# Kernel tuning notes

Measured on AMD Instinct MI355X. Metric: run time of the kernel, lower is better.

## Reference

```python
import jax, jax.numpy as jnp
import numpy as np

B, S, HID = 1, 4096, 4096
H, KV, D = 32, 8, 128
NUM_LANDMARKS = 64
LOCAL_WINDOW = 128          # window size in fast path
HW = LOCAL_WINDOW // 2      # half window = 64 (also used as block size)
ROPE_THETA = 10000.0
SCALE = 1.0 / np.sqrt(D)


def setup_inputs() -> dict:
    key = jax.random.key(0)
    k1, k2, k3, k4, k5 = jax.random.split(key, 5)
    return {
        "hidden_states": jax.random.normal(k1, (B, S, HID), dtype=jnp.float32),
        "wq": jax.random.normal(k2, (HID, H * D), dtype=jnp.float32) * 0.02,
        "wk": jax.random.normal(k3, (HID, KV * D), dtype=jnp.float32) * 0.02,
        "wv": jax.random.normal(k4, (HID, KV * D), dtype=jnp.float32) * 0.02,
        "wo": jax.random.normal(k5, (H * D, HID), dtype=jnp.float32) * 0.02,
    }


def _rope(x):
    # x: [B, h, S, D]; standard llama RoPE with rotate_half
    pos = jnp.arange(S, dtype=jnp.float32)
    inv_freq = 1.0 / (ROPE_THETA ** (jnp.arange(0, D, 2, dtype=jnp.float32) / D))
    freqs = pos[:, None] * inv_freq[None, :]              # [S, D/2]
    emb = jnp.concatenate([freqs, freqs], axis=-1)        # [S, D]
    cos, sin = jnp.cos(emb), jnp.sin(emb)
    x1, x2 = x[..., : D // 2], x[..., D // 2:]
    rot = jnp.concatenate([-x2, x1], axis=-1)
    return x * cos + rot * sin


def _ssa_fast(q, k, v):
    # q,k,v: [B, H, S, D] (kv already repeated to H heads). Causal, no dropout.
    nblk = S // HW  # block size == half window == 64
    # ---- local sliding-window attention (block-banded, honors sparsity) ----
    qb = q.reshape(B, H, nblk, HW, D)
    # pad keys/values by HW zeros on both sides (matches torch F.pad with 0)
    kp = jnp.pad(k, ((0, 0), (0, 0), (HW, HW), (0, 0)))
    vp = jnp.pad(v, ((0, 0), (0, 0), (HW, HW), (0, 0)))
    kpb = kp.reshape(B, H, nblk + 2, HW, D)
    vpb = vp.reshape(B, H, nblk + 2, HW, D)
    # each query block n sees key blocks n-1, n, n+1 (in padded coords: n, n+1, n+2)
    kb = jnp.concatenate([kpb[:, :, :nblk], kpb[:, :, 1:nblk + 1], kpb[:, :, 2:nblk + 2]], axis=3)  # [B,H,nblk,3*HW,D]
    vb = jnp.concatenate([vpb[:, :, :nblk], vpb[:, :, 1:nblk + 1], vpb[:, :, 2:nblk + 2]], axis=3)
    scores = jnp.einsum("bhnqd,bhnkd->bhnqk", qb, kb) * SCALE  # [B,H,nblk,HW,3*HW]
    # relative key position: rel = (j - HW) - i; window membership rel in [-HW, HW-1],
    # causal keeps rel <= 0  =>  i <= j <= i + HW. Left zero-padding stays attendable
    # (score 0), exactly like the torch unfold-over-zero-pad implementation.
    i_idx = jnp.arange(HW)[:, None]
    j_idx = jnp.arange(3 * HW)[None, :]
    mask = (j_idx >= i_idx) & (j_idx <= i_idx + HW)  # [HW, 3*HW]
    scores = jnp.where(mask, scores, -jnp.inf)
    w = jax.nn.softmax(scores, axis=-1)
    local_out = jnp.einsum("bhnqk,bhnkd->bhnqd", w, vb).reshape(B, H, S, D)
    # ---- global landmark attention ----
    stride = S // NUM_LANDMARKS
    lm_idx = jnp.arange(0, S, stride)[:NUM_LANDMARKS]         # [L]
    lk = k[:, :, lm_idx, :]                                   # [B,H,L,D]
    lv = v[:, :, lm_idx, :]
    ls = jnp.einsum("bhqd,bhkd->bhqk", q, lk) * SCALE         # [B,H,S,L]
    lm_mask = jnp.arange(S)[:, None] < lm_idx[None, :]        # future landmarks masked
    ls = jnp.where(lm_mask[None, None], -jnp.inf, ls)
    lw = jax.nn.softmax(ls, axis=-1)
    global_out = jnp.einsum("bhqk,bhkd->bhqd", lw, lv)
    return 0.7 * local_out + 0.3 * global_out


def reference(hidden_states, wq, wk, wv, wo):
    q = (hidden_states @ wq).reshape(B, S, H, D).transpose(0, 2, 1, 3)   # [B,H,S,D]
    k = (hidden_states @ wk).reshape(B, S, KV, D).transpose(0, 2, 1, 3)  # [B,KV,S,D]
    v = (hidden_states @ wv).reshape(B, S, KV, D).transpose(0, 2, 1, 3)
    q = _rope(q)
    k = _rope(k)
    groups = H // KV
    k = jnp.repeat(k, groups, axis=1)  # repeat_interleave over heads
    v = jnp.repeat(v, groups, axis=1)
    attn = _ssa_fast(q, k, v)                                 # [B,H,S,D]
    out = attn.transpose(0, 2, 1, 3).reshape(B, S, H * D) @ wo
    return out
```

## Files before the change

### kernel.cpp

```cpp
#include <hip/hip_runtime.h>
#include <hip/hip_bf16.h>


typedef short bf16x8 __attribute__((ext_vector_type(8)));
typedef float f32x4 __attribute__((ext_vector_type(4)));
using bf16 = __hip_bfloat16;

#define S_LEN 4096
#define HIDN  4096
#define NH    32
#define NKV   8
#define DH    128
#define NBLK  64
#define SCALE 0.08838834764831845f

__device__ __forceinline__ void gload16(const bf16* g, bf16* l) {
  __builtin_amdgcn_global_load_lds(
      (const __attribute__((address_space(1))) unsigned int*)g,
      (__attribute__((address_space(3))) unsigned int*)l, 16, 0, 0);
}

__global__ void k_detect(const unsigned short* __restrict__ w,
                         int* __restrict__ flag) {
  int t = threadIdx.x;
  unsigned short u = w[t];
  int e = (u >> 7) & 0xFF;
  int bad = (e >= 134) ? 1 : 0;
  __shared__ int cnt;
  if (t == 0) cnt = 0;
  __syncthreads();
  atomicAdd(&cnt, bad);
  __syncthreads();
  if (t == 0) flag[0] = (cnt > 32) ? 1 : 0;
}

__global__ void k_cvt(const void* __restrict__ in, bf16* __restrict__ out,
                      const int* __restrict__ flagp, int n8) {
  int i = blockIdx.x * blockDim.x + threadIdx.x;
  if (i >= n8) return;
  if (*flagp) {
    const float4* p = (const float4*)in + (size_t)i * 2;
    float4 a = p[0], b = p[1];
    alignas(16) bf16 v[8] = {__float2bfloat16(a.x), __float2bfloat16(a.y),
                             __float2bfloat16(a.z), __float2bfloat16(a.w),
                             __float2bfloat16(b.x), __float2bfloat16(b.y),
                             __float2bfloat16(b.z), __float2bfloat16(b.w)};
    *(uint4*)(out + (size_t)i * 8) = *(const uint4*)v;
  } else {
    ((uint4*)out)[i] = ((const uint4*)in)[i];
  }
}

__global__ __launch_bounds__(256) void k_tcvt(const void* __restrict__ w_,
                                              bf16* __restrict__ wt,
                                              const int* __restrict__ flagp,
                                              int K, int N) {
  __shared__ bf16 tile[64][66];
  const bool f32 = *flagp != 0;
  const int k0 = blockIdx.x * 64, n0 = blockIdx.y * 64;
  const int t = threadIdx.x;
  const int r = t >> 2, c16 = (t & 3) * 16;
  if (f32) {
    const float* src = (const float*)w_ + (size_t)(k0 + r) * N + n0 + c16;
    float4 a = ((const float4*)src)[0], b = ((const float4*)src)[1];
    float4 c = ((const float4*)src)[2], d = ((const float4*)src)[3];
    bf16* dst = &tile[r][c16];
    dst[0] = __float2bfloat16(a.x);  dst[1] = __float2bfloat16(a.y);
    dst[2] = __float2bfloat16(a.z);  dst[3] = __float2bfloat16(a.w);
    dst[4] = __float2bfloat16(b.x);  dst[5] = __float2bfloat16(b.y);
    dst[6] = __float2bfloat16(b.z);  dst[7] = __float2bfloat16(b.w);
    dst[8] = __float2bfloat16(c.x);  dst[9] = __float2bfloat16(c.y);
    dst[10] = __float2bfloat16(c.z); dst[11] = __float2bfloat16(c.w);
    dst[12] = __float2bfloat16(d.x); dst[13] = __float2bfloat16(d.y);
    dst[14] = __float2bfloat16(d.z); dst[15] = __float2bfloat16(d.w);
  } else {
    const bf16* src = (const bf16*)w_ + (size_t)(k0 + r) * N + n0 + c16;
    uint4 a = ((const uint4*)src)[0], b = ((const uint4*)src)[1];
    *(uint4*)(&tile[r][c16]) = a;
    *(uint4*)(&tile[r][c16 + 8]) = b;
  }
  __syncthreads();
  alignas(16) bf16 v[16];
#pragma unroll
  for (int j = 0; j < 16; j++) v[j] = tile[c16 + j][r];
  bf16* dst = wt + (size_t)(n0 + r) * K + k0 + c16;
  ((uint4*)dst)[0] = ((const uint4*)v)[0];
  ((uint4*)dst)[1] = ((const uint4*)v)[1];
}

__global__ __launch_bounds__(256) void k_gemm(
    const bf16* __restrict__ A, const bf16* __restrict__ BT,
    void* __restrict__ outQ, void* __restrict__ outK, void* __restrict__ outV,
    const int* __restrict__ flagp, int M, int N, int K, int kind) {
  __shared__ bf16 Al[128 * 64];
  __shared__ bf16 Bl[128 * 64];
  const int m0 = blockIdx.x * 128, n0 = blockIdx.y * 128;
  const int t = threadIdx.x;
  const int wid = t >> 6, lane = t & 63, quad = lane >> 4, l16 = lane & 15;
  const int wr = (wid >> 1) * 64, wc = (wid & 1) * 64;
  const int srow = wid * 32 + (lane >> 3);
  const int sgof = (((lane & 7) ^ (lane >> 3))) * 8;
  const int slof = (lane & 7) * 8;
  f32x4 acc[4][4] = {};

  for (int kb = 0; kb < K; kb += 64) {
#pragma unroll
    for (int p = 0; p < 4; p++) {
      int row = srow + p * 8;
      gload16(A + (size_t)(m0 + row) * K + kb + sgof, Al + row * 64 + slof);
      gload16(BT + (size_t)(n0 + row) * K + kb + sgof, Bl + row * 64 + slof);
    }
    __syncthreads();
#pragma unroll
    for (int kk = 0; kk < 64; kk += 32) {
      bf16x8 af[4], bfr[4];
#pragma unroll
      for (int i = 0; i < 4; i++) {
        int sb = (((kk >> 3) + quad) ^ (l16 & 7)) * 8;
        af[i] = *(const bf16x8*)(&Al[(wr + i * 16 + l16) * 64 + sb]);
        bfr[i] = *(const bf16x8*)(&Bl[(wc + i * 16 + l16) * 64 + sb]);
      }
#pragma unroll
      for (int mt = 0; mt < 4; mt++)
#pragma unroll
        for (int nt = 0; nt < 4; nt++)
          acc[mt][nt] = __builtin_amdgcn_mfma_f32_16x16x32_bf16(
              af[mt], bfr[nt], acc[mt][nt], 0, 0, 0);
    }
    __syncthreads();
  }
  const bool storeF32 = (kind == 1) && (*flagp != 0);
#pragma unroll
  for (int mt = 0; mt < 4; mt++)
#pragma unroll
    for (int nt = 0; nt < 4; nt++)
#pragma unroll
      for (int r = 0; r < 4; r++) {
        int m = m0 + wr + mt * 16 + quad * 4 + r;
        int n = n0 + wc + nt * 16 + l16;
        float v = acc[mt][nt][r];
        if (kind == 1) {
          if (storeF32)
            ((float*)outQ)[(size_t)m * N + n] = v;
          else
            ((bf16*)outQ)[(size_t)m * N + n] = __float2bfloat16(v);
        } else {
          bf16* Co;
          if (n < 4096)
            Co = (bf16*)outQ + (size_t)m * 4096 + n;
          else if (n < 5120)
            Co = (bf16*)outK + (size_t)m * 1024 + (n - 4096);
          else
            Co = (bf16*)outV + (size_t)m * 1024 + (n - 5120);
          *Co = __float2bfloat16(v);
        }
      }
}

__global__ void k_rope(bf16* __restrict__ Q, bf16* __restrict__ Kb,
                       int totalQ, int total) {
  int idx = blockIdx.x * blockDim.x + threadIdx.x;
  if (idx >= total) return;
  bf16* x;
  int nheads, li;
  if (idx < totalQ) { x = Q; nheads = NH; li = idx; }
  else { x = Kb; nheads = NKV; li = idx - totalQ; }
  int j = li & 63;
  int sh = li >> 6;
  int s = sh / nheads;
  float invf = (float)exp(-(double)j * (9.210340371976184 / 64.0));
  float ang = (float)s * invf;
  float sn, cs;
  sincosf(ang, &sn, &cs);
  bf16* p = x + (size_t)sh * DH;
  float x1 = __bfloat162float(p[j]);
  float x2 = __bfloat162float(p[j + 64]);
  p[j]      = __float2bfloat16(x1 * cs - x2 * sn);
  p[j + 64] = __float2bfloat16(x2 * cs + x1 * sn);
}

__global__ __launch_bounds__(256) void k_attn(const bf16* __restrict__ Q,
                                              const bf16* __restrict__ Kk,
                                              const bf16* __restrict__ V,
                                              bf16* __restrict__ O) {
  const int nb = blockIdx.x;
  const int h = blockIdx.y;
  const int kvh = h >> 2;
  const int t = threadIdx.x;
  const int wid = t >> 6, lane = t & 63, quad = lane >> 4, l16 = lane & 15;

  __shared__ bf16 Qs[64 * 136];
  __shared__ bf16 kvb[128 * 136];
  __shared__ bf16 PLs[64 * 72];

  const int srow16 = t >> 4, soff = (t & 15) * 8;

#pragma unroll
  for (int p = 0; p < 4; p++) {
    int row = p * 16 + srow16;
    *(uint4*)(&Qs[row * 136 + soff]) =
        *(const uint4*)(Q + ((size_t)(nb * 64 + row) * NH + h) * DH + soff);
  }

  auto stageK = [&](int basePos, int posStride) {
#pragma unroll
    for (int p = 0; p < 4; p++) {
      int row = p * 16 + srow16;
      int pos = basePos + row * posStride;
      uint4 val = make_uint4(0u, 0u, 0u, 0u);
      if (pos >= 0)
        val = *(const uint4*)(Kk + ((size_t)pos * NKV + kvh) * DH + soff);
      *(uint4*)(&kvb[row * 136 + soff]) = val;
    }
  };

  auto stageVt = [&](int basePos, int posStride) {
#pragma unroll
    for (int p = 0; p < 4; p++) {
      int key = p * 16 + srow16;
      int pos = basePos + key * posStride;
      uint4 tv = make_uint4(0u, 0u, 0u, 0u);
      if (pos >= 0)
        tv = *(const uint4*)(V + ((size_t)pos * NKV + kvh) * DH + soff);
      const bf16* tmp = (const bf16*)&tv;
#pragma unroll
      for (int jj = 0; jj < 8; jj++)
        kvb[(soff + jj) * 72 + key] = tmp[jj];
    }
  };

  f32x4 sc[8] = {};
  f32x4 slm[4] = {};

  auto scoreStep = [&](f32x4* dst) {
#pragma unroll
    for (int kk = 0; kk < 128; kk += 32) {
      bf16x8 a = *(const bf16x8*)(&Qs[(wid * 16 + l16) * 136 + kk + quad * 8]);
#pragma unroll
      for (int nt = 0; nt < 4; nt++) {
        bf16x8 b =
            *(const bf16x8*)(&kvb[(nt * 16 + l16) * 136 + kk + quad * 8]);
        dst[nt] = __builtin_amdgcn_mfma_f32_16x16x32_bf16(a, b, dst[nt], 0, 0, 0);
      }
    }
  };

  stageK(nb * 64 - 64, 1);
  __syncthreads();
  scoreStep(&sc[0]);
  __syncthreads();
  stageK(nb * 64, 1);
  __syncthreads();
  scoreStep(&sc[4]);
  __syncthreads();
  stageK(0, 64);
  __syncthreads();
  scoreStep(&slm[0]);
  __syncthreads();

  float invL[4], invG[4];
#pragma unroll
  for (int r = 0; r < 4; r++) {
    const int i = wid * 16 + quad * 4 + r;
    float mx = -1e30f;
#pragma unroll
    for (int nt = 0; nt < 8; nt++) {
      int j = nt * 16 + l16;
      float s = sc[nt][r] * SCALE;
      if (j < i || j > i + 64) s = -1e30f;
      sc[nt][r] = s;
      mx = fmaxf(mx, s);
    }
#pragma unroll
    for (int m = 1; m <= 8; m <<= 1) mx = fmaxf(mx, __shfl_xor(mx, m, 64));
    float sum = 0.f;
#pragma unroll
    for (int nt = 0; nt < 8; nt++) {
      float e = __expf(sc[nt][r] - mx);
      sc[nt][r] = e;
      sum += e;
    }
#pragma unroll
    for (int m = 1; m <= 8; m <<= 1) sum += __shfl_xor(sum, m, 64);
    invL[r] = 0.7f / sum;

    float mg = -1e30f;
#pragma unroll
    for (int nt = 0; nt < 4; nt++) {
      int l = nt * 16 + l16;
      float s = slm[nt][r] * SCALE;
      if (l > nb) s = -1e30f;
      slm[nt][r] = s;
      mg = fmaxf(mg, s);
    }
#pragma unroll
    for (int m = 1; m <= 8; m <<= 1) mg = fmaxf(mg, __shfl_xor(mg, m, 64));
    float sg = 0.f;
#pragma unroll
    for (int nt = 0; nt < 4; nt++) {
      float e = __expf(slm[nt][r] - mg);
      slm[nt][r] = e;
      sg += e;
    }
#pragma unroll
    for (int m = 1; m <= 8; m <<= 1) sg += __shfl_xor(sg, m, 64);
    invG[r] = 0.3f / sg;
  }

#pragma unroll
  for (int nt = 0; nt < 8; nt++)
#pragma unroll
    for (int r = 0; r < 4; r++)
      Qs[(wid * 16 + quad * 4 + r) * 136 + nt * 16 + l16] =
          __float2bfloat16(sc[nt][r]);
#pragma unroll
  for (int nt = 0; nt < 4; nt++)
#pragma unroll
    for (int r = 0; r < 4; r++)
      PLs[(wid * 16 + quad * 4 + r) * 72 + nt * 16 + l16] =
          __float2bfloat16(slm[nt][r]);
  stageVt(nb * 64 - 64, 1);
  __syncthreads();

  f32x4 accO[8] = {};
  f32x4 accG[8] = {};
  auto pvStep = [&](f32x4* dst, const bf16* Pbase, int pstride, int colbase) {
#pragma unroll
    for (int kk = 0; kk < 64; kk += 32) {
      bf16x8 a = *(const bf16x8*)(&Pbase[(wid * 16 + l16) * pstride + colbase +
                                         kk + quad * 8]);
#pragma unroll
      for (int nt = 0; nt < 8; nt++) {
        bf16x8 b = *(const bf16x8*)(&kvb[(nt * 16 + l16) * 72 + kk + quad * 8]);
        dst[nt] = __builtin_amdgcn_mfma_f32_16x16x32_bf16(a, b, dst[nt], 0, 0, 0);
      }
    }
  };
  pvStep(accO, Qs, 136, 0);
  __syncthreads();
  stageVt(nb * 64, 1);
  __syncthreads();
  pvStep(accO, Qs, 136, 64);
  __syncthreads();
  stageVt(0, 64);
  __syncthreads();
  pvStep(accG, PLs, 72, 0);

#pragma unroll
  for (int nt = 0; nt < 8; nt++)
#pragma unroll
    for (int r = 0; r < 4; r++) {
      int q = nb * 64 + wid * 16 + quad * 4 + r;
      int d = nt * 16 + l16;
      float v = accO[nt][r] * invL[r] + accG[nt][r] * invG[r];
      O[((size_t)q * NH + h) * DH + d] = __float2bfloat16(v);
    }
}

extern "C" void kernel_launch(void* const* d_in, const int* in_sizes, int n_in,
                              void* d_out, int out_size, void* d_ws,
                              size_t ws_size, hipStream_t stream) {
  const void* X  = d_in[0];
  const void* wq = d_in[1];
  const void* wk = d_in[2];
  const void* wv = d_in[3];
  const void* wo = d_in[4];

  char* ws = (char*)d_ws;
  int* flag = (int*)ws;
  bf16* Xb   = (bf16*)(ws + 256);
  bf16* Wcat = Xb + (size_t)S_LEN * HIDN;
  bf16* Qb   = Wcat + (size_t)6144 * HIDN;
  bf16* Kb   = Qb + (size_t)S_LEN * HIDN;
  bf16* Vb   = Kb + (size_t)S_LEN * 1024;
  bf16* At   = Xb;
  bf16* WoT  = Wcat;

  k_detect<<<1, 256, 0, stream>>>((const unsigned short*)wq, flag);

  k_cvt<<<(S_LEN * HIDN / 8 + 255) / 256, 256, 0, stream>>>(
      X, Xb, flag, S_LEN * HIDN / 8);
  k_tcvt<<<dim3(HIDN / 64, HIDN / 64), 256, 0, stream>>>(
      wq, Wcat, flag, HIDN, HIDN);
  k_tcvt<<<dim3(HIDN / 64, 1024 / 64), 256, 0, stream>>>(
      wk, Wcat + (size_t)4096 * HIDN, flag, HIDN, 1024);
  k_tcvt<<<dim3(HIDN / 64, 1024 / 64), 256, 0, stream>>>(
      wv, Wcat + (size_t)5120 * HIDN, flag, HIDN, 1024);

  k_gemm<<<dim3(S_LEN / 128, 6144 / 128), 256, 0, stream>>>(
      Xb, Wcat, Qb, Kb, Vb, flag, S_LEN, 6144, HIDN, 0);

  int totalQ = S_LEN * NH * 64, total = totalQ + S_LEN * NKV * 64;
  k_rope<<<(total + 255) / 256, 256, 0, stream>>>(Qb, Kb, totalQ, total);

  k_attn<<<dim3(NBLK, NH), 256, 0, stream>>>(Qb, Kb, Vb, At);

  k_tcvt<<<dim3(HIDN / 64, HIDN / 64), 256, 0, stream>>>(
      wo, WoT, flag, HIDN, HIDN);

  k_gemm<<<dim3(S_LEN / 128, HIDN / 128), 256, 0, stream>>>(
      At, WoT, d_out, nullptr, nullptr, flag, S_LEN, HIDN, HIDN, 1);
}
```

Baseline: 760.4 us.

## Rewrite GEMM as 256x256-tile, 512-thread, double-buffered pipelined kernel

Replaces the 128x128 single-buffered GEMM with a 256x256 tile computed by 8 waves. It double-buffers LDS in half-K stages, issues async global-to-LDS loads interleaved with MFMA phases, and controls them with explicit vmcnt waits and barriers. It also adds XCD-aware block remapping, an LDS swizzle and MFMA priority hints. The aim is to hide global-load latency behind compute and raise data reuse in both projection GEMMs. The cost is 128KB of LDS and a larger register footprint, so fewer blocks fit on each CU.

```diff
diff --git a/kernel.cpp b/kernel.cpp
--- a/kernel.cpp
+++ b/kernel.cpp
@@ -88,57 +88,112 @@
   ((uint4*)dst)[1] = ((const uint4*)v)[1];
 }
 
-__global__ __launch_bounds__(256) void k_gemm(
+#define WAITV(N) asm volatile("s_waitcnt vmcnt(" #N ")" ::: "memory")
+#define BARRIER()                                \
+  do {                                           \
+    asm volatile("" ::: "memory");               \
+    __builtin_amdgcn_s_barrier();                \
+    asm volatile("" ::: "memory");               \
+  } while (0)
+
+__global__ __launch_bounds__(512, 2) void k_gemm(
     const bf16* __restrict__ A, const bf16* __restrict__ BT,
     void* __restrict__ outQ, void* __restrict__ outK, void* __restrict__ outV,
     const int* __restrict__ flagp, int M, int N, int K, int kind) {
-  __shared__ bf16 Al[128 * 64];
-  __shared__ bf16 Bl[128 * 64];
-  const int m0 = blockIdx.x * 128, n0 = blockIdx.y * 128;
+  __shared__ __align__(16) bf16 lds[65536];
+  const int NT = K >> 6;
+  const int mb = M >> 8;
+  const int nwg = mb * (N >> 8);
+  const int bid = blockIdx.y * gridDim.x + blockIdx.x;
+  const int lin = (bid & 7) * (nwg >> 3) + (bid >> 3);
+  const int m0 = (lin % mb) << 8;
+  const int n0 = (lin / mb) << 8;
   const int t = threadIdx.x;
   const int wid = t >> 6, lane = t & 63, quad = lane >> 4, l16 = lane & 15;
-  const int wr = (wid >> 1) * 64, wc = (wid & 1) * 64;
-  const int srow = wid * 32 + (lane >> 3);
-  const int sgof = (((lane & 7) ^ (lane >> 3))) * 8;
-  const int slof = (lane & 7) * 8;
-  f32x4 acc[4][4] = {};
-
-  for (int kb = 0; kb < K; kb += 64) {
-#pragma unroll
-    for (int p = 0; p < 4; p++) {
-      int row = srow + p * 8;
-      gload16(A + (size_t)(m0 + row) * K + kb + sgof, Al + row * 64 + slof);
-      gload16(BT + (size_t)(n0 + row) * K + kb + sgof, Bl + row * 64 + slof);
-    }
-    __syncthreads();
-#pragma unroll
-    for (int kk = 0; kk < 64; kk += 32) {
-      bf16x8 af[4], bfr[4];
-#pragma unroll
-      for (int i = 0; i < 4; i++) {
-        int sb = (((kk >> 3) + quad) ^ (l16 & 7)) * 8;
-        af[i] = *(const bf16x8*)(&Al[(wr + i * 16 + l16) * 64 + sb]);
-        bfr[i] = *(const bf16x8*)(&Bl[(wc + i * 16 + l16) * 64 + sb]);
-      }
-#pragma unroll
-      for (int mt = 0; mt < 4; mt++)
-#pragma unroll
-        for (int nt = 0; nt < 4; nt++)
-          acc[mt][nt] = __builtin_amdgcn_mfma_f32_16x16x32_bf16(
-              af[mt], bfr[nt], acc[mt][nt], 0, 0, 0);
-    }
-    __syncthreads();
-  }
+  const int wr = wid >> 2, wc = wid & 3;
+  const int sw = (quad ^ ((l16 >> 1) & 3)) * 8;
+
+  f32x4 acc[8][4] = {};
+  bf16x8 a[4], bfr[4];
+
+  auto stageHalf = [&](int g) {
+    const int kt = g >> 2, j = g & 3;
+    const int buf = kt & 1, isB = j & 1, kh = j >> 1;
+    const bf16* src = isB ? BT : A;
+    const int r0 = isB ? n0 : m0;
+    const int base = (isB ? 32768 : 0) + buf * 16384 + kh * 8192;
+    const int kcol = kt * 64 + kh * 32;
+#pragma unroll
+    for (int p = 0; p < 2; p++) {
+      int u = p * 512 + t;
+      int r = u >> 2;
+      int gb = (u & 3) ^ ((r >> 1) & 3);
+      gload16(src + (size_t)(r0 + r) * K + kcol + gb * 8, &lds[base + u * 8]);
+    }
+  };
+
+#define READS(kt, KH, MH)                                                     \
+  {                                                                           \
+    const int abase = ((kt) & 1) * 16384 + (KH) * 8192;                       \
+    _Pragma("unroll") for (int i = 0; i < 4; i++) a[i] =                      \
+        *(const bf16x8*)&lds[abase +                                          \
+                             (wr * 128 + ((MH) * 4 + i) * 16 + l16) * 32 +    \
+                             sw];                                             \
+    if ((MH) == 0) {                                                          \
+      const int bbase = 32768 + ((kt) & 1) * 16384 + (KH) * 8192;             \
+      _Pragma("unroll") for (int j = 0; j < 4; j++) bfr[j] =                  \
+          *(const bf16x8*)&lds[bbase + (wc * 64 + j * 16 + l16) * 32 + sw];   \
+    }                                                                         \
+  }
+
+#define MFMAS(MH)                                                             \
+  {                                                                           \
+    __builtin_amdgcn_s_setprio(1);                                            \
+    _Pragma("unroll") for (int i = 0; i < 4; i++)                             \
+        _Pragma("unroll") for (int j = 0; j < 4; j++) acc[(MH) * 4 + i][j] =  \
+            __builtin_amdgcn_mfma_f32_16x16x32_bf16(                          \
+                a[i], bfr[j], acc[(MH) * 4 + i][j], 0, 0, 0);                 \
+    __builtin_amdgcn_s_setprio(0);                                            \
+  }
+
+  stageHalf(0); stageHalf(1); stageHalf(2); stageHalf(3);
+  stageHalf(4); stageHalf(5);
+  WAITV(8);
+  BARRIER();
+
+  const int G = 4 * NT;
+  for (int kt = 0; kt < NT; ++kt) {
+    const int g = 4 * kt + 6;
+    READS(kt, 0, 0);
+    if (g < G) stageHalf(g);
+    MFMAS(0);
+    BARRIER();
+    READS(kt, 0, 1);
+    if (g + 1 < G) stageHalf(g + 1);
+    MFMAS(1);
+    if (kt < NT - 1) { WAITV(8); } else { WAITV(0); }
+    BARRIER();
+    READS(kt, 1, 0);
+    if (g + 2 < G) stageHalf(g + 2);
+    MFMAS(0);
+    BARRIER();
+    READS(kt, 1, 1);
+    if (g + 3 < G) stageHalf(g + 3);
+    MFMAS(1);
+    if (kt < NT - 2) { WAITV(8); } else if (kt == NT - 2) { WAITV(4); }
+    BARRIER();
+  }
+
   const bool storeF32 = (kind == 1) && (*flagp != 0);
 #pragma unroll
-  for (int mt = 0; mt < 4; mt++)
-#pragma unroll
-    for (int nt = 0; nt < 4; nt++)
+  for (int i = 0; i < 8; i++)
+#pragma unroll
+    for (int j = 0; j < 4; j++)
 #pragma unroll
       for (int r = 0; r < 4; r++) {
-        int m = m0 + wr + mt * 16 + quad * 4 + r;
-        int n = n0 + wc + nt * 16 + l16;
-        float v = acc[mt][nt][r];
+        int m = m0 + wr * 128 + i * 16 + quad * 4 + r;
+        int n = n0 + wc * 64 + j * 16 + l16;
+        float v = acc[i][j][r];
         if (kind == 1) {
           if (storeF32)
             ((float*)outQ)[(size_t)m * N + n] = v;
@@ -387,7 +442,7 @@
   k_tcvt<<<dim3(HIDN / 64, 1024 / 64), 256, 0, stream>>>(
       wv, Wcat + (size_t)5120 * HIDN, flag, HIDN, 1024);
 
-  k_gemm<<<dim3(S_LEN / 128, 6144 / 128), 256, 0, stream>>>(
+  k_gemm<<<dim3(S_LEN / 256, 6144 / 256), 512, 0, stream>>>(
       Xb, Wcat, Qb, Kb, Vb, flag, S_LEN, 6144, HIDN, 0);
 
   int totalQ = S_LEN * NH * 64, total = totalQ + S_LEN * NKV * 64;
@@ -398,6 +453,6 @@
   k_tcvt<<<dim3(HIDN / 64, HIDN / 64), 256, 0, stream>>>(
       wo, WoT, flag, HIDN, HIDN);
 
-  k_gemm<<<dim3(S_LEN / 128, HIDN / 128), 256, 0, stream>>>(
+  k_gemm<<<dim3(S_LEN / 256, HIDN / 256), 512, 0, stream>>>(
       At, WoT, d_out, nullptr, nullptr, flag, S_LEN, HIDN, HIDN, 1);
 }
```

Result: faster. 722.1 us (-5.0%).
